# Optimization experiments

Hardware: AMD Instinct MI355X
Metric: run time of the kernel (lower is better)

The kernel has to match this reference:

```python
import jax, jax.numpy as jnp
import numpy as np

N = 4096   # number of nodes
E = 4096   # number of hyperedges
F_IN = 128
F_OUT = 128
AVG_DEG = 32.0


def setup_inputs() -> dict:
    key = jax.random.key(0)
    k_x, k_h, k_w = jax.random.split(key, 3)
    X = jax.random.normal(k_x, (N, F_IN), dtype=jnp.float32)
    # Binary incidence matrix with average node degree ~AVG_DEG
    H = (jax.random.uniform(k_h, (N, E)) < (AVG_DEG / E)).astype(jnp.float32)
    # Diagonal degree matrices (clamped >= 1 so they are invertible)
    dv = jnp.maximum(H.sum(axis=1), 1.0)   # [N] vertex degrees
    de = jnp.maximum(H.sum(axis=0), 1.0)   # [E] hyperedge degrees
    D_v = jnp.diag(dv)                     # [N, N]
    D_e = jnp.diag(de)                     # [E, E]
    # Xavier-uniform weight
    limit = float(np.sqrt(6.0 / (F_IN + F_OUT)))
    W = jax.random.uniform(k_w, (F_IN, F_OUT), minval=-limit, maxval=limit,
                           dtype=jnp.float32)
    return {"X": X, "H": H, "D_v": D_v, "D_e": D_e, "W": W}


def reference(X, H, D_v, D_e, W):
    # Faithful to torch: generic matrix inverse of the (diagonal) degree matrices
    D_v_inv = jnp.linalg.inv(D_v)          # [N, N]
    D_e_inv = jnp.linalg.inv(D_e)          # [E, E]
    theta = X @ W                          # [N, F_out]
    coeff = D_v_inv @ H                    # [N, E]
    coeff = coeff @ D_e_inv                # [N, E]
    coeff = coeff @ H.T                    # [N, N]
    return coeff @ theta                   # [N, F_out]
```

## Files before the change

### kernel.cpp

```cpp
#include <hip/hip_runtime.h>

constexpr int N = 4096;
constexpr int E = 4096;
constexpr int F = 128;
constexpr int MAXL = 128;
constexpr int DIAG_LD = 4097;

__device__ __forceinline__ ushort f2bf_rne(float x) {
    union { float f; unsigned u; } v; v.f = x;
    return (ushort)((v.u + 0x7FFFu + ((v.u >> 16) & 1u)) >> 16);
}

__global__ __launch_bounds__(256) void k_theta(const float* __restrict__ X,
                                               const float* __restrict__ W,
                                               ushort* __restrict__ theta_bf) {
    __shared__ float Xs[16][F];
    const int t = threadIdx.x;
    const int r0 = blockIdx.x * 16;
    #pragma unroll
    for (int i = 0; i < 2; ++i) {
        const int idx = i * 256 + t;
        const int rr = idx >> 5, cc = (idx & 31) * 4;
        *(float4*)&Xs[rr][cc] = *(const float4*)&X[(size_t)(r0 + rr) * F + cc];
    }
    __syncthreads();
    const int f = t & 127, half = t >> 7;
    float acc[8];
    #pragma unroll
    for (int i = 0; i < 8; ++i) acc[i] = 0.f;
    #pragma unroll 4
    for (int k = 0; k < F; ++k) {
        const float w = W[k * F + f];
        #pragma unroll
        for (int i = 0; i < 8; ++i) acc[i] += Xs[half * 8 + i][k] * w;
    }
    #pragma unroll
    for (int i = 0; i < 8; ++i)
        theta_bf[(size_t)(r0 + half * 8 + i) * F + f] = f2bf_rne(acc[i]);
}

__global__ __launch_bounds__(256) void k_build(const float* __restrict__ H,
                                               int* __restrict__ row_cnt,
                                               ushort* __restrict__ row_list,
                                               int* __restrict__ col_cnt,
                                               ushort* __restrict__ col_list) {
    __shared__ int lcnt[4];
    const int t = threadIdx.x, wave = t >> 6, lane = t & 63;
    if (t < 4) lcnt[t] = 0;
    __syncthreads();
    const int r = blockIdx.x * 4 + wave;
    const float* Hr = H + (size_t)r * E;
    for (int j = 0; j < 4; ++j) {
        uint4 v[4];
        #pragma unroll
        for (int q = 0; q < 4; ++q)
            v[q] = *(const uint4*)&Hr[((j * 4 + q) * 64 + lane) * 4];
        #pragma unroll
        for (int q = 0; q < 4; ++q) {
            if (v[q].x | v[q].y | v[q].z | v[q].w) {
                const int c0 = ((j * 4 + q) * 64 + lane) * 4;
                const uint vv[4] = {v[q].x, v[q].y, v[q].z, v[q].w};
                #pragma unroll
                for (int c = 0; c < 4; ++c) {
                    if (vv[c]) {
                        const int e = c0 + c;
                        const int p = atomicAdd(&lcnt[wave], 1);
                        if (p < MAXL) row_list[(size_t)r * MAXL + p] = (ushort)e;
                        const int g = atomicAdd(&col_cnt[e], 1);
                        if (g < MAXL) col_list[(size_t)e * MAXL + g] = (ushort)r;
                    }
                }
            }
        }
    }
    __syncthreads();
    if (lane == 0) row_cnt[r] = lcnt[wave] < MAXL ? lcnt[wave] : MAXL;
}

template <bool OUT_BF16>
__global__ __launch_bounds__(256) void k_spmm(const int* __restrict__ cnt,
                                              const ushort* __restrict__ list,
                                              const ushort* __restrict__ Vin,
                                              const float* __restrict__ Dmat,
                                              void* __restrict__ Vout) {
    __shared__ ushort sIdx[4][MAXL];
    const int t = threadIdx.x, wave = t >> 6, lane = t & 63;
    const int r = blockIdx.x * 4 + wave;
    *(ushort2*)&sIdx[wave][lane * 2] =
        *(const ushort2*)&list[(size_t)r * MAXL + lane * 2];
    int c = cnt[r]; c = c < MAXL ? c : MAXL;
    const float dscale = 1.0f / Dmat[(size_t)r * DIAG_LD];
    __syncthreads();
    const char* vb = (const char*)Vin;
    float a0 = 0.f, a1 = 0.f;
    int i = 0;
    for (; i + 8 <= c; i += 8) {
        uint v[8];
        #pragma unroll
        for (int j = 0; j < 8; ++j)
            v[j] = *(const uint*)(vb + ((int)sIdx[wave][i + j] * 256 + lane * 4));
        #pragma unroll
        for (int j = 0; j < 8; ++j) {
            a0 += __uint_as_float((v[j] & 0xffffu) << 16);
            a1 += __uint_as_float((v[j] >> 16) << 16);
        }
    }
    for (; i < c; ++i) {
        const uint v = *(const uint*)(vb + ((int)sIdx[wave][i] * 256 + lane * 4));
        a0 += __uint_as_float((v & 0xffffu) << 16);
        a1 += __uint_as_float((v >> 16) << 16);
    }
    a0 *= dscale; a1 *= dscale;
    if (OUT_BF16) {
        ushort2 o; o.x = f2bf_rne(a0); o.y = f2bf_rne(a1);
        *(ushort2*)((ushort*)Vout + (size_t)r * F + lane * 2) = o;
    } else {
        float2 o; o.x = a0; o.y = a1;
        *(float2*)((float*)Vout + (size_t)r * F + lane * 2) = o;
    }
}

extern "C" void kernel_launch(void* const* d_in, const int* in_sizes, int n_in,
                              void* d_out, int out_size, void* d_ws, size_t ws_size,
                              hipStream_t stream) {
    const float* X  = (const float*)d_in[0];
    const float* H  = (const float*)d_in[1];
    const float* Dv = (const float*)d_in[2];
    const float* De = (const float*)d_in[3];
    const float* W  = (const float*)d_in[4];
    float* out = (float*)d_out;
    char* ws = (char*)d_ws;

    ushort* theta    = (ushort*)ws;
    ushort* M        = (ushort*)(ws + (size_t)1 * 1024 * 1024);
    ushort* row_list = (ushort*)(ws + (size_t)2 * 1024 * 1024);
    ushort* col_list = (ushort*)(ws + (size_t)3 * 1024 * 1024);
    int*    row_cnt  = (int*)   (ws + (size_t)4 * 1024 * 1024);
    int*    col_cnt  = row_cnt + N;

    hipMemsetAsync(col_cnt, 0, (size_t)E * sizeof(int), stream);

    k_theta<<<dim3(N / 16), dim3(256), 0, stream>>>(X, W, theta);
    k_build<<<dim3(N / 4), dim3(256), 0, stream>>>(H, row_cnt, row_list,
                                                   col_cnt, col_list);
    k_spmm<true ><<<dim3(E / 4), dim3(256), 0, stream>>>(col_cnt, col_list,
                                                         theta, De, M);
    k_spmm<false><<<dim3(N / 4), dim3(256), 0, stream>>>(row_cnt, row_list,
                                                         M, Dv, out);
}
```

Measured before the change: 215.0 us.

## Build column lists via bitmask transpose instead of global atomics

The incidence scan now emits a per-row bitmask of H alongside the row lists. A second kernel transposes that bitmask in shared memory to build the per-hyperedge column lists. This removes the global atomicAdd on col_cnt and the scattered col_list writes, and also drops the memset. In exchange it adds an extra launch and a 2 MB bitmask round trip, and pass2 runs only 64 blocks, so parallelism is low.

```diff
diff --git a/kernel.cpp b/kernel.cpp
--- a/kernel.cpp
+++ b/kernel.cpp
@@ -39,42 +39,78 @@
         theta_bf[(size_t)(r0 + half * 8 + i) * F + f] = f2bf_rne(acc[i]);
 }
 
-__global__ __launch_bounds__(256) void k_build(const float* __restrict__ H,
+__global__ __launch_bounds__(256) void k_pass1(const float* __restrict__ H,
+                                               unsigned long long* __restrict__ BM,
                                                int* __restrict__ row_cnt,
-                                               ushort* __restrict__ row_list,
-                                               int* __restrict__ col_cnt,
-                                               ushort* __restrict__ col_list) {
+                                               ushort* __restrict__ row_list) {
+    __shared__ ushort sL[4][MAXL];
     __shared__ int lcnt[4];
     const int t = threadIdx.x, wave = t >> 6, lane = t & 63;
-    if (t < 4) lcnt[t] = 0;
-    __syncthreads();
+    if (lane == 0) lcnt[wave] = 0;
     const int r = blockIdx.x * 4 + wave;
     const float* Hr = H + (size_t)r * E;
-    for (int j = 0; j < 4; ++j) {
-        uint4 v[4];
+    #pragma unroll
+    for (int half = 0; half < 2; ++half) {
+        uint4 v[8];
         #pragma unroll
-        for (int q = 0; q < 4; ++q)
-            v[q] = *(const uint4*)&Hr[((j * 4 + q) * 64 + lane) * 4];
+        for (int q = 0; q < 8; ++q)
+            v[q] = *(const uint4*)&Hr[((half * 8 + q) * 64 + lane) * 4];
+        unsigned long long wreg = 0;
         #pragma unroll
-        for (int q = 0; q < 4; ++q) {
-            if (v[q].x | v[q].y | v[q].z | v[q].w) {
-                const int c0 = ((j * 4 + q) * 64 + lane) * 4;
-                const uint vv[4] = {v[q].x, v[q].y, v[q].z, v[q].w};
-                #pragma unroll
-                for (int c = 0; c < 4; ++c) {
-                    if (vv[c]) {
-                        const int e = c0 + c;
-                        const int p = atomicAdd(&lcnt[wave], 1);
-                        if (p < MAXL) row_list[(size_t)r * MAXL + p] = (ushort)e;
-                        const int g = atomicAdd(&col_cnt[e], 1);
-                        if (g < MAXL) col_list[(size_t)e * MAXL + g] = (ushort)r;
-                    }
+        for (int q = 0; q < 8; ++q) {
+            const int i = half * 8 + q;
+            const uint vv[4] = {v[q].x, v[q].y, v[q].z, v[q].w};
+            #pragma unroll
+            for (int c = 0; c < 4; ++c) {
+                const unsigned long long m = __ballot(vv[c] != 0u);
+                const int widx = q * 4 + c;
+                if (lane == widx) wreg = m;
+                if (vv[c]) {
+                    const int p = atomicAdd(&lcnt[wave], 1);
+                    if (p < MAXL) sL[wave][p] = (ushort)(i * 256 + 4 * lane + c);
                 }
             }
         }
+        if (lane < 32)
+            BM[(size_t)r * 64 + half * 32 + lane] = wreg;
+    }
+    const int cnt = lcnt[wave] < MAXL ? lcnt[wave] : MAXL;
+    ((uint*)&row_list[(size_t)r * MAXL])[lane] = ((const uint*)sL[wave])[lane];
+    if (lane == 0) row_cnt[r] = cnt;
+}
+
+__global__ __launch_bounds__(512) void k_pass2(
+        const unsigned long long* __restrict__ BM,
+        int* __restrict__ col_cnt,
+        ushort* __restrict__ col_list) {
+    __shared__ ushort sL[64][MAXL];
+    __shared__ int cnt[64];
+    const int t = threadIdx.x, wave = t >> 6, lane = t & 63;
+    const int wc = blockIdx.x;
+    if (t < 64) cnt[t] = 0;
+    __syncthreads();
+    unsigned long long w8[8];
+    #pragma unroll
+    for (int j = 0; j < 8; ++j)
+        w8[j] = BM[(size_t)(wave * 512 + j * 64 + lane) * 64 + wc];
+    #pragma unroll
+    for (int j = 0; j < 8; ++j) {
+        unsigned long long m = w8[j];
+        const ushort row = (ushort)(wave * 512 + j * 64 + lane);
+        while (m) {
+            const int b = __builtin_ctzll(m); m &= m - 1;
+            const int p = atomicAdd(&cnt[b], 1);
+            if (p < MAXL) sL[b][p] = row;
+        }
     }
     __syncthreads();
-    if (lane == 0) row_cnt[r] = lcnt[wave] < MAXL ? lcnt[wave] : MAXL;
+    const int el = t >> 3, ch = t & 7;
+    const int e = (wc >> 2) * 256 + 4 * el + (wc & 3);
+    const uint4* src = (const uint4*)sL[el];
+    uint4* dst = (uint4*)&col_list[(size_t)e * MAXL];
+    dst[ch * 2 + 0] = src[ch * 2 + 0];
+    dst[ch * 2 + 1] = src[ch * 2 + 1];
+    if (ch == 0) col_cnt[e] = cnt[el] < MAXL ? cnt[el] : MAXL;
 }
 
 template <bool OUT_BF16>
@@ -132,17 +168,17 @@
     char* ws = (char*)d_ws;
 
     ushort* theta    = (ushort*)ws;
+    unsigned long long* BM =
+        (unsigned long long*)(ws + (size_t)1 * 1024 * 1024);
     ushort* M        = (ushort*)(ws + (size_t)1 * 1024 * 1024);
-    ushort* row_list = (ushort*)(ws + (size_t)2 * 1024 * 1024);
-    ushort* col_list = (ushort*)(ws + (size_t)3 * 1024 * 1024);
-    int*    row_cnt  = (int*)   (ws + (size_t)4 * 1024 * 1024);
+    ushort* row_list = (ushort*)(ws + (size_t)3 * 1024 * 1024);
+    ushort* col_list = (ushort*)(ws + (size_t)4 * 1024 * 1024);
+    int*    row_cnt  = (int*)   (ws + (size_t)5 * 1024 * 1024);
     int*    col_cnt  = row_cnt + N;
 
-    hipMemsetAsync(col_cnt, 0, (size_t)E * sizeof(int), stream);
-
     k_theta<<<dim3(N / 16), dim3(256), 0, stream>>>(X, W, theta);
-    k_build<<<dim3(N / 4), dim3(256), 0, stream>>>(H, row_cnt, row_list,
-                                                   col_cnt, col_list);
+    k_pass1<<<dim3(N / 4), dim3(256), 0, stream>>>(H, BM, row_cnt, row_list);
+    k_pass2<<<dim3(64), dim3(512), 0, stream>>>(BM, col_cnt, col_list);
     k_spmm<true ><<<dim3(E / 4), dim3(256), 0, stream>>>(col_cnt, col_list,
                                                          theta, De, M);
     k_spmm<false><<<dim3(N / 4), dim3(256), 0, stream>>>(row_cnt, row_list,
```

Measured after the change: 207.1 us. -3.6%, faster.
